# Kernel optimization log

Hardware: AMD Instinct MI355X
Metric: run time of the kernel (lower is better)

The kernel has to match this reference:

```python
import jax, jax.numpy as jnp
import numpy as np

NUM_MIX = 50
CMD_LEN = 4
ARG_LEN = 6
MIX_TEMP = 0.0001
GAUSS_TEMP = 0.0001


def setup_inputs() -> dict:
    key = jax.random.key(0)
    k1, k2, k3 = jax.random.split(key, 3)
    S, B, H = 51, 2048, 1024
    out_ch = CMD_LEN + ARG_LEN * NUM_MIX * 3  # 904
    decoder_output = jax.random.normal(k1, (S, B, H), dtype=jnp.float32)
    W = jax.random.normal(k2, (out_ch, H), dtype=jnp.float32) * (1.0 / np.sqrt(H))
    b = jax.random.normal(k3, (out_ch,), dtype=jnp.float32) * 0.01
    return {"decoder_output": decoder_output, "W": W, "b": b}


def reference(decoder_output, W, b):
    S, B, H = decoder_output.shape
    # fc: [S,B,H] @ [H,out_ch] + b  -> [S,B,904]
    ret = jnp.einsum('sbh,oh->sbo', decoder_output, W) + b

    key = jax.random.key(42)
    k_cmd, k_mix, k_gauss = jax.random.split(key, 3)

    # command: temperature softmax + categorical sample + one-hot
    cmd_logits = ret[..., :CMD_LEN] / MIX_TEMP  # [S,B,4]
    cmd_idx = jax.random.categorical(k_cmd, cmd_logits)  # [S,B]
    command = jax.nn.one_hot(cmd_idx, CMD_LEN, dtype=decoder_output.dtype)

    # MDN coefficients over flattened rows: N = S*B*ARG_LEN
    arguments = ret[..., CMD_LEN:].reshape(-1, 3 * NUM_MIX)  # [N,150]
    logmix = arguments[:, :NUM_MIX]
    mean = arguments[:, NUM_MIX:2 * NUM_MIX]
    logstd = arguments[:, 2 * NUM_MIX:]
    logmix = logmix - jax.nn.logsumexp(logmix, axis=-1, keepdims=True)

    # sample mixture component with temperature (softmax of logmix/temp)
    mix_idx = jax.random.categorical(k_mix, logmix / MIX_TEMP)  # [N]

    # vectorized gather of chosen mean/logstd (replaces per-row python loop)
    chosen_mean = jnp.take_along_axis(mean, mix_idx[:, None], axis=1)[:, 0]
    chosen_logstd = jnp.take_along_axis(logstd, mix_idx[:, None], axis=1)[:, 0]

    noise = jax.random.normal(k_gauss, chosen_mean.shape, dtype=chosen_mean.dtype)
    noise = noise * np.sqrt(GAUSS_TEMP)
    args_out = chosen_mean + jnp.exp(chosen_logstd) * noise  # [N]
    args_out = args_out.reshape(-1, B, ARG_LEN)  # [S,B,6]

    return jnp.concatenate([command, args_out], axis=-1)  # [S,B,10]
```

## Files before the change

kernel.cpp:

```cpp
#include <hip/hip_runtime.h>
#include <stdint.h>
#include <math.h>

#pragma clang fp contract(off)

#define M_TOTAL 104448
#define N_OUT   904
#define K_DIM   1024

#define BM 64
#define BN 64
#define BK 16

__host__ __device__ inline uint32_t rotl32(uint32_t x, int r) {
    return (x << r) | (x >> (32 - r));
}

__host__ __device__ inline void threefry2x32(uint32_t k0, uint32_t k1,
                                             uint32_t x0, uint32_t x1,
                                             uint32_t& o0, uint32_t& o1) {
    uint32_t ks2 = k0 ^ k1 ^ 0x1BD11BDAu;
    x0 += k0; x1 += k1;
#define R4(a,b,c,d) \
    x0 += x1; x1 = rotl32(x1,(a)); x1 ^= x0; \
    x0 += x1; x1 = rotl32(x1,(b)); x1 ^= x0; \
    x0 += x1; x1 = rotl32(x1,(c)); x1 ^= x0; \
    x0 += x1; x1 = rotl32(x1,(d)); x1 ^= x0;
    R4(13,15,26,6)  x0 += k1;  x1 += ks2 + 1u;
    R4(17,29,16,24) x0 += ks2; x1 += k0  + 2u;
    R4(13,15,26,6)  x0 += k0;  x1 += k1  + 3u;
    R4(17,29,16,24) x0 += k1;  x1 += ks2 + 4u;
    R4(13,15,26,6)  x0 += ks2; x1 += k0  + 5u;
#undef R4
    o0 = x0; o1 = x1;
}

__device__ inline uint32_t random_bits_part(uint32_t k0, uint32_t k1, uint32_t idx) {
    uint32_t o0, o1;
    threefry2x32(k0, k1, 0u, idx, o0, o1);
    return o0 ^ o1;
}

__device__ inline float bits_to_unit(uint32_t bits) {
    return __uint_as_float((bits >> 9) | 0x3f800000u) - 1.0f;
}

__device__ inline float logf_cr(float x) { return (float)log((double)x); }
__device__ inline float expf_cr(float x) { return (float)exp((double)x); }

__device__ inline float gumbel_at(uint32_t k0, uint32_t k1, uint32_t idx) {
    float f = bits_to_unit(random_bits_part(k0, k1, idx));
    float u = fmaxf(f, 1.17549435e-38f);
    float t = logf_cr(u);
    return -logf_cr(-t);
}

__device__ inline float erfinv_xla(float x) {
    float w = -log1pf(-x * x);
    float p;
    if (w < 5.0f) {
        w = w - 2.5f;
        p = 2.81022636e-08f;
        p = 3.43273939e-07f  + p * w;
        p = -3.5233877e-06f  + p * w;
        p = -4.39150654e-06f + p * w;
        p = 0.00021858087f   + p * w;
        p = -0.00125372503f  + p * w;
        p = -0.00417768164f  + p * w;
        p = 0.246640727f     + p * w;
        p = 1.50140941f      + p * w;
    } else {
        w = sqrtf(w) - 3.0f;
        p = -0.000200214257f;
        p = 0.000100950558f  + p * w;
        p = 0.00134934322f   + p * w;
        p = -0.00367342844f  + p * w;
        p = 0.00573950773f   + p * w;
        p = -0.0076224613f   + p * w;
        p = 0.00943887047f   + p * w;
        p = 1.00167406f      + p * w;
        p = 2.83297682f      + p * w;
    }
    return p * x;
}

__global__ __launch_bounds__(256) void gemm_np_sse(
    const float* __restrict__ X,
    const float* __restrict__ W,
    const float* __restrict__ bias,
    float* __restrict__ ret,
    int rows)
{
    __shared__ float As[BK][BM];
    __shared__ float Bs[BK][BN];

    const int t  = threadIdx.x;
    const int tx = t & 15;
    const int ty = t >> 4;
    const int m0 = blockIdx.y * BM;
    const int n0 = blockIdx.x * BN;

    const int lrow = t >> 2;
    const int lc4  = (t & 3) * 4;

    float acc[4][4][4];
#pragma unroll
    for (int i = 0; i < 4; i++)
#pragma unroll
        for (int j = 0; j < 4; j++)
#pragma unroll
            for (int l = 0; l < 4; l++) acc[i][j][l] = 0.0f;

    for (int k0 = 0; k0 < K_DIM; k0 += BK) {
        float4 av = *(const float4*)(X + (size_t)(m0 + lrow) * K_DIM + k0 + lc4);
        float4 bv;
        int go = n0 + lrow;
        if (go < N_OUT) bv = *(const float4*)(W + (size_t)go * K_DIM + k0 + lc4);
        else            bv = make_float4(0.f, 0.f, 0.f, 0.f);

        __syncthreads();
        As[lc4 + 0][lrow] = av.x; As[lc4 + 1][lrow] = av.y;
        As[lc4 + 2][lrow] = av.z; As[lc4 + 3][lrow] = av.w;
        Bs[lc4 + 0][lrow] = bv.x; Bs[lc4 + 1][lrow] = bv.y;
        Bs[lc4 + 2][lrow] = bv.z; Bs[lc4 + 3][lrow] = bv.w;
        __syncthreads();

#pragma unroll
        for (int q = 3; q >= 0; q--) {
#pragma unroll
            for (int kk = 0; kk < 4; kk++) {
                const int k = q * 4 + kk;
                float4 af = *(const float4*)&As[k][ty * 4];
                float4 bf = *(const float4*)&Bs[k][tx * 4];
                acc[0][0][kk] = af.x * bf.x + acc[0][0][kk];
                acc[0][1][kk] = af.x * bf.y + acc[0][1][kk];
                acc[0][2][kk] = af.x * bf.z + acc[0][2][kk];
                acc[0][3][kk] = af.x * bf.w + acc[0][3][kk];
                acc[1][0][kk] = af.y * bf.x + acc[1][0][kk];
                acc[1][1][kk] = af.y * bf.y + acc[1][1][kk];
                acc[1][2][kk] = af.y * bf.z + acc[1][2][kk];
                acc[1][3][kk] = af.y * bf.w + acc[1][3][kk];
                acc[2][0][kk] = af.z * bf.x + acc[2][0][kk];
                acc[2][1][kk] = af.z * bf.y + acc[2][1][kk];
                acc[2][2][kk] = af.z * bf.z + acc[2][2][kk];
                acc[2][3][kk] = af.z * bf.w + acc[2][3][kk];
                acc[3][0][kk] = af.w * bf.x + acc[3][0][kk];
                acc[3][1][kk] = af.w * bf.y + acc[3][1][kk];
                acc[3][2][kk] = af.w * bf.z + acc[3][2][kk];
                acc[3][3][kk] = af.w * bf.w + acc[3][3][kk];
            }
        }
    }

#pragma unroll
    for (int i = 0; i < 4; i++) {
        int m = m0 + ty * 4 + i;
        if (m >= rows) continue;
#pragma unroll
        for (int j = 0; j < 4; j++) {
            int o = n0 + tx * 4 + j;
            if (o >= N_OUT) continue;
            float res = (acc[i][j][0] + acc[i][j][1]) + (acc[i][j][2] + acc[i][j][3]);
            ret[(size_t)m * N_OUT + o] = res + bias[o];
        }
    }
}

__global__ __launch_bounds__(256) void sample_kernel(
    const float* __restrict__ ret,
    float* __restrict__ out,
    int m0_global, int rows,
    uint32_t kc0, uint32_t kc1,
    uint32_t km0, uint32_t km1,
    uint32_t kg0, uint32_t kg1)
{
    const int lane = threadIdx.x & 63;
    const int wid  = threadIdx.x >> 6;
    const int rloc = blockIdx.x * 4 + wid;
    if (rloc >= rows) return;
    const int m = m0_global + rloc;

    const float* r = ret + (size_t)rloc * N_OUT;
    float* o = out + (size_t)m * 10;

    const float LO = __uint_as_float(0xBF7FFFFFu);
    const float SQRT2 = __uint_as_float(0x3FB504F3u);

    {
        float v; int idx = lane;
        if (lane < 4) {
            float g = gumbel_at(kc0, kc1, (uint32_t)(m * 4 + lane));
            v = r[lane] / 0.0001f + g;
        } else {
            v = -INFINITY;
        }
#pragma unroll
        for (int off = 1; off < 64; off <<= 1) {
            float v2 = __shfl_xor(v, off);
            int   i2 = __shfl_xor(idx, off);
            if (v2 > v || (v2 == v && i2 < idx)) { v = v2; idx = i2; }
        }
        if (lane < 4) o[lane] = (lane == idx) ? 1.0f : 0.0f;
    }

    for (int a = 0; a < 6; a++) {
        const float* base = r + 4 + a * 150;
        float l = (lane < 50) ? base[lane] : -INFINITY;

        float mx = l;
#pragma unroll
        for (int off = 1; off < 64; off <<= 1) mx = fmaxf(mx, __shfl_xor(mx, off));

        float e = (lane < 50) ? expf_cr(l - mx) : 0.0f;

        float rj = (lane < 8) ? e : 0.0f;
#pragma unroll
        for (int tstep = 1; tstep <= 5; tstep++) {
            float ev = __shfl(e, (lane & 7) + 8 * tstep);
            if (lane < 8) rj = rj + ev;
        }
        float r0 = __shfl(rj, 0), r1 = __shfl(rj, 1), r2 = __shfl(rj, 2), r3 = __shfl(rj, 3);
        float r4 = __shfl(rj, 4), r5 = __shfl(rj, 5), r6 = __shfl(rj, 6), r7 = __shfl(rj, 7);
        float s = ((r0 + r1) + (r2 + r3)) + ((r4 + r5) + (r6 + r7));
        s = s + __shfl(e, 48);
        s = s + __shfl(e, 49);

        float lse = logf_cr(s) + mx;

        float vv; int ii = lane;
        if (lane < 50) {
            float g = gumbel_at(km0, km1, (uint32_t)((m * 6 + a) * 50 + lane));
            vv = (l - lse) / 0.0001f + g;
        } else {
            vv = -INFINITY;
        }
#pragma unroll
        for (int off = 1; off < 64; off <<= 1) {
            float v2 = __shfl_xor(vv, off);
            int   i2 = __shfl_xor(ii, off);
            if (v2 > vv || (v2 == vv && i2 < ii)) { vv = v2; ii = i2; }
        }

        if (lane == 0) {
            float mean = base[50 + ii];
            float lstd = base[100 + ii];
            uint32_t eidx = (uint32_t)(m * 6 + a);
            float f = bits_to_unit(random_bits_part(kg0, kg1, eidx));
            float val = f * 2.0f + LO;
            val = fmaxf(LO, val);
            float nrm = SQRT2 * erfinv_xla(val);
            float noise = nrm * 0.01f;
            o[4 + a] = mean + expf_cr(lstd) * noise;
        }
    }
}

extern "C" void kernel_launch(void* const* d_in, const int* in_sizes, int n_in,
                              void* d_out, int out_size, void* d_ws, size_t ws_size,
                              hipStream_t stream) {
    const float* X    = (const float*)d_in[0];
    const float* W    = (const float*)d_in[1];
    const float* bias = (const float*)d_in[2];
    float* out = (float*)d_out;
    float* ws  = (float*)d_ws;

    uint32_t kc0, kc1, km0, km1, kg0, kg1;
    threefry2x32(0u, 42u, 0u, 0u, kc0, kc1);
    threefry2x32(0u, 42u, 0u, 1u, km0, km1);
    threefry2x32(0u, 42u, 0u, 2u, kg0, kg1);

    const size_t rowBytes = (size_t)N_OUT * sizeof(float);
    size_t rowsCap = ws_size / rowBytes;
    int chunk = (rowsCap >= (size_t)M_TOTAL) ? M_TOTAL : (int)rowsCap;
    chunk -= chunk % BM;
    if (chunk <= 0) chunk = BM;

    const int gx = (N_OUT + BN - 1) / BN;

    for (int m0 = 0; m0 < M_TOTAL; m0 += chunk) {
        int rows = M_TOTAL - m0;
        if (rows > chunk) rows = chunk;
        dim3 ggrid(gx, rows / BM);
        gemm_np_sse<<<ggrid, 256, 0, stream>>>(X + (size_t)m0 * K_DIM, W, bias, ws, rows);
        sample_kernel<<<dim3(rows / 4), 256, 0, stream>>>(ws, out, m0, rows,
                                                          kc0, kc1, km0, km1, kg0, kg1);
    }
}
```

Before: 6.108 ms.

## Use 128x64 tiles with paired threads splitting K over 8x8 microtiles

Doubles the GEMM block tile in M and assigns each pair of threads an 8x8 output microtile, with the two threads splitting each 4-wide K group and combining partial sums via a lane shuffle. This raises FMA-per-LDS-load reuse and halves the number of B-tile reloads across blocks. It costs more registers per thread (128 accumulators), which may lower occupancy, and it changes the floating-point summation order.

```diff
diff --git a/kernel.cpp b/kernel.cpp
--- a/kernel.cpp
+++ b/kernel.cpp
@@ -8,7 +8,7 @@
 #define N_OUT   904
 #define K_DIM   1024
 
-#define BM 64
+#define BM 128
 #define BN 64
 #define BK 16
 
@@ -84,7 +84,7 @@
     return p * x;
 }
 
-__global__ __launch_bounds__(256) void gemm_np_sse(
+__global__ __launch_bounds__(256) void gemm_np_sse_pair(
     const float* __restrict__ X,
     const float* __restrict__ W,
     const float* __restrict__ bias,
@@ -94,74 +94,73 @@
     __shared__ float As[BK][BM];
     __shared__ float Bs[BK][BN];
 
-    const int t  = threadIdx.x;
-    const int tx = t & 15;
-    const int ty = t >> 4;
-    const int m0 = blockIdx.y * BM;
-    const int n0 = blockIdx.x * BN;
-
-    const int lrow = t >> 2;
-    const int lc4  = (t & 3) * 4;
-
-    float acc[4][4][4];
-#pragma unroll
-    for (int i = 0; i < 4; i++)
-#pragma unroll
-        for (int j = 0; j < 4; j++)
-#pragma unroll
-            for (int l = 0; l < 4; l++) acc[i][j][l] = 0.0f;
+    const int t    = threadIdx.x;
+    const int h    = t & 1;
+    const int pair = t >> 1;
+    const int pm   = pair >> 3;
+    const int pn   = pair & 7;
+    const int m0   = blockIdx.y * BM;
+    const int n0   = blockIdx.x * BN;
+
+    const int sm  = t >> 2;
+    const int skq = t & 3;
+
+    float acc[8][8][2];
+#pragma unroll
+    for (int i = 0; i < 8; i++)
+#pragma unroll
+        for (int j = 0; j < 8; j++) { acc[i][j][0] = 0.0f; acc[i][j][1] = 0.0f; }
 
     for (int k0 = 0; k0 < K_DIM; k0 += BK) {
-        float4 av = *(const float4*)(X + (size_t)(m0 + lrow) * K_DIM + k0 + lc4);
-        float4 bv;
-        int go = n0 + lrow;
-        if (go < N_OUT) bv = *(const float4*)(W + (size_t)go * K_DIM + k0 + lc4);
-        else            bv = make_float4(0.f, 0.f, 0.f, 0.f);
+        float4 a0 = *(const float4*)(X + (size_t)(m0 + sm)      * K_DIM + k0 + skq * 4);
+        float4 a1 = *(const float4*)(X + (size_t)(m0 + sm + 64) * K_DIM + k0 + skq * 4);
+        float4 b0;
+        int gn = n0 + sm;
+        if (gn < N_OUT) b0 = *(const float4*)(W + (size_t)gn * K_DIM + k0 + skq * 4);
+        else            b0 = make_float4(0.f, 0.f, 0.f, 0.f);
 
         __syncthreads();
-        As[lc4 + 0][lrow] = av.x; As[lc4 + 1][lrow] = av.y;
-        As[lc4 + 2][lrow] = av.z; As[lc4 + 3][lrow] = av.w;
-        Bs[lc4 + 0][lrow] = bv.x; Bs[lc4 + 1][lrow] = bv.y;
-        Bs[lc4 + 2][lrow] = bv.z; Bs[lc4 + 3][lrow] = bv.w;
+        As[skq * 4 + 0][sm]      = a0.x; As[skq * 4 + 1][sm]      = a0.y;
+        As[skq * 4 + 2][sm]      = a0.z; As[skq * 4 + 3][sm]      = a0.w;
+        As[skq * 4 + 0][sm + 64] = a1.x; As[skq * 4 + 1][sm + 64] = a1.y;
+        As[skq * 4 + 2][sm + 64] = a1.z; As[skq * 4 + 3][sm + 64] = a1.w;
+        Bs[skq * 4 + 0][sm]      = b0.x; Bs[skq * 4 + 1][sm]      = b0.y;
+        Bs[skq * 4 + 2][sm]      = b0.z; Bs[skq * 4 + 3][sm]      = b0.w;
         __syncthreads();
 
 #pragma unroll
         for (int q = 3; q >= 0; q--) {
 #pragma unroll
-            for (int kk = 0; kk < 4; kk++) {
-                const int k = q * 4 + kk;
-                float4 af = *(const float4*)&As[k][ty * 4];
-                float4 bf = *(const float4*)&Bs[k][tx * 4];
-                acc[0][0][kk] = af.x * bf.x + acc[0][0][kk];
-                acc[0][1][kk] = af.x * bf.y + acc[0][1][kk];
-                acc[0][2][kk] = af.x * bf.z + acc[0][2][kk];
-                acc[0][3][kk] = af.x * bf.w + acc[0][3][kk];
-                acc[1][0][kk] = af.y * bf.x + acc[1][0][kk];
-                acc[1][1][kk] = af.y * bf.y + acc[1][1][kk];
-                acc[1][2][kk] = af.y * bf.z + acc[1][2][kk];
-                acc[1][3][kk] = af.y * bf.w + acc[1][3][kk];
-                acc[2][0][kk] = af.z * bf.x + acc[2][0][kk];
-                acc[2][1][kk] = af.z * bf.y + acc[2][1][kk];
-                acc[2][2][kk] = af.z * bf.z + acc[2][2][kk];
-                acc[2][3][kk] = af.z * bf.w + acc[2][3][kk];
-                acc[3][0][kk] = af.w * bf.x + acc[3][0][kk];
-                acc[3][1][kk] = af.w * bf.y + acc[3][1][kk];
-                acc[3][2][kk] = af.w * bf.z + acc[3][2][kk];
-                acc[3][3][kk] = af.w * bf.w + acc[3][3][kk];
+            for (int cc = 0; cc < 2; cc++) {
+                const int k = q * 4 + (h ? 2 : 0) + cc;
+                float4 av0 = *(const float4*)&As[k][pm * 8];
+                float4 av1 = *(const float4*)&As[k][pm * 8 + 4];
+                float4 bv0 = *(const float4*)&Bs[k][pn * 8];
+                float4 bv1 = *(const float4*)&Bs[k][pn * 8 + 4];
+                float a[8] = {av0.x, av0.y, av0.z, av0.w, av1.x, av1.y, av1.z, av1.w};
+                float b[8] = {bv0.x, bv0.y, bv0.z, bv0.w, bv1.x, bv1.y, bv1.z, bv1.w};
+#pragma unroll
+                for (int i = 0; i < 8; i++)
+#pragma unroll
+                    for (int j = 0; j < 8; j++)
+                        acc[i][j][cc] = a[i] * b[j] + acc[i][j][cc];
             }
         }
     }
 
 #pragma unroll
-    for (int i = 0; i < 4; i++) {
-        int m = m0 + ty * 4 + i;
-        if (m >= rows) continue;
-#pragma unroll
-        for (int j = 0; j < 4; j++) {
-            int o = n0 + tx * 4 + j;
-            if (o >= N_OUT) continue;
-            float res = (acc[i][j][0] + acc[i][j][1]) + (acc[i][j][2] + acc[i][j][3]);
-            ret[(size_t)m * N_OUT + o] = res + bias[o];
+    for (int i = 0; i < 8; i++) {
+#pragma unroll
+        for (int j = 0; j < 8; j++) {
+            float tmine  = acc[i][j][0] + acc[i][j][1];
+            float tother = __shfl_xor(tmine, 1);
+            if (h == 0) {
+                float res = tmine + tother;
+                int m = m0 + pm * 8 + i;
+                int o = n0 + pn * 8 + j;
+                if (o < N_OUT)
+                    ret[(size_t)m * N_OUT + o] = res + bias[o];
+            }
         }
     }
 }
@@ -281,7 +280,7 @@
         int rows = M_TOTAL - m0;
         if (rows > chunk) rows = chunk;
         dim3 ggrid(gx, rows / BM);
-        gemm_np_sse<<<ggrid, 256, 0, stream>>>(X + (size_t)m0 * K_DIM, W, bias, ws, rows);
+        gemm_np_sse_pair<<<ggrid, 256, 0, stream>>>(X + (size_t)m0 * K_DIM, W, bias, ws, rows);
         sample_kernel<<<dim3(rows / 4), 256, 0, stream>>>(ws, out, m0, rows,
                                                           kc0, kc1, km0, km1, kg0, kg1);
     }
```

Result: slower. 7.226 ms (+18.3%).
